# Kernel optimization log

Measured on AMD Instinct MI355X. Metric: run time of the kernel, lower is better.

## Reference

```python
import jax, jax.numpy as jnp
import numpy as np

BITS = 8
KH, KW = 3, 3
STRIDE = (1, 1)
PAD = (1, 1)


def _quantize_signed_symmetric(x, bits=BITS):
    # Per-tensor symmetric quantization: scale = max|x| / qmax, q = clip(round(x/scale)).
    qmax = float(2 ** (bits - 1) - 1)
    scale = jnp.max(jnp.abs(x)) / qmax
    q = jnp.clip(jnp.round(x / scale), -qmax, qmax)
    return q, scale


def _unfold(x, kh, kw, stride, pad):
    # torch.nn.functional.unfold: output [B, C*kh*kw, Hout*Wout], feature order (c, kh, kw).
    B, C, H, W = x.shape
    sh, sw = stride
    ph, pw = pad
    Hout = (H + 2 * ph - kh) // sh + 1
    Wout = (W + 2 * pw - kw) // sw + 1
    xp = jnp.pad(x, ((0, 0), (0, 0), (ph, ph), (pw, pw)))
    patches = []
    for i in range(kh):  # small fixed loop over kernel taps (9 iters)
        for j in range(kw):
            patches.append(
                xp[:, :, i:i + (Hout - 1) * sh + 1:sh, j:j + (Wout - 1) * sw + 1:sw]
            )
    # [B, C, kh*kw, Hout, Wout] -> [B, C*kh*kw, Hout*Wout]
    p = jnp.stack(patches, axis=2)
    return p.reshape(B, C * kh * kw, Hout * Wout), Hout, Wout


def setup_inputs() -> dict:
    key = jax.random.key(0)
    k1, k2, k3 = jax.random.split(key, 3)
    x = jax.random.normal(k1, (8, 32, 224, 224), dtype=jnp.float32)
    weight = jax.random.normal(k2, (32, 32, 3, 3), dtype=jnp.float32)
    bias = jax.random.normal(k3, (32,), dtype=jnp.float32)
    return {"x": x, "weight": weight, "bias": bias}


def reference(x, weight, bias):
    Cout = weight.shape[0]
    B = x.shape[0]
    qw, w_scale = _quantize_signed_symmetric(weight)           # values are exact small ints
    x_unf, Hout, Wout = _unfold(x, KH, KW, STRIDE, PAD)        # [B, K, L], K=Cin*kh*kw
    qx, x_scale = _quantize_signed_symmetric(x_unf)
    qw_flat = qw.reshape(Cout, -1)                             # [Cout, K]
    # Integer GEMM done in fp32: |sum| <= K*127^2 = 288*16129 < 2^24, so exact.
    out = jnp.einsum("ok,bkl->bol", qw_flat, qx)               # [B, Cout, L]
    out = out * (x_scale * w_scale)                            # dequantize
    out = out + bias[None, :, None]
    return out.reshape(B, Cout, Hout, Wout)
```

## Files before the change

### kernel.cpp

```cpp
#include <hip/hip_runtime.h>
#include <hip/hip_bf16.h>
#include <stdint.h>


typedef short short8 __attribute__((ext_vector_type(8)));
typedef float f32x4  __attribute__((ext_vector_type(4)));

#define CIN   32
#define COUT  32
#define HH    224
#define WW    224
#define NB    8
#define QMAXF 127.0f
#define PP    226

#define RED_BLOCKS 1024
#define PF_OFF  16
#define QW_OFF  8192
#define QX_OFF  32768
#define QX_BYTES ((size_t)NB * PP * PP * CIN * 2)


__global__ __launch_bounds__(256) void k_prep(const float* __restrict__ x, int n4,
                                              const float* __restrict__ wgt,
                                              unsigned* __restrict__ ws) {
    const int tid = threadIdx.x;
    __shared__ float red[4];
    if (blockIdx.x < RED_BLOCKS) {
        const float4* x4 = (const float4*)x;
        float m = 0.f;
        for (int i = blockIdx.x * 256 + tid; i < n4; i += RED_BLOCKS * 256) {
            float4 v = x4[i];
            m = fmaxf(m, fmaxf(fmaxf(fabsf(v.x), fabsf(v.y)), fmaxf(fabsf(v.z), fabsf(v.w))));
        }
        #pragma unroll
        for (int off = 32; off >= 1; off >>= 1) m = fmaxf(m, __shfl_xor(m, off));
        if ((tid & 63) == 0) red[tid >> 6] = m;
        __syncthreads();
        if (tid == 0)
            ((float*)ws)[PF_OFF + blockIdx.x] =
                fmaxf(fmaxf(red[0], red[1]), fmaxf(red[2], red[3]));
    } else {
        float m = 0.f;
        for (int i = tid; i < COUT * CIN * 9; i += 256) m = fmaxf(m, fabsf(wgt[i]));
        #pragma unroll
        for (int off = 32; off >= 1; off >>= 1) m = fmaxf(m, __shfl_xor(m, off));
        if ((tid & 63) == 0) red[tid >> 6] = m;
        __syncthreads();
        const float mw = fmaxf(fmaxf(red[0], red[1]), fmaxf(red[2], red[3]));
        const float wscale = mw / QMAXF;
        if (tid == 0) ws[1] = __float_as_uint(wscale);
        ushort* qw = (ushort*)((char*)ws + QW_OFF);
        for (int e = tid; e < COUT * 288; e += 256) {
            const int co = e / 288, k = e % 288;
            const int t = k >> 5, ci = k & 31;
            const int kh = t / 3, kw = t % 3;
            const float v = wgt[((co * CIN + ci) * 3 + kh) * 3 + kw];
            float q = rintf(v / wscale);
            q = fminf(fmaxf(q, -QMAXF), QMAXF);
            qw[e] = (ushort)(__float_as_uint(q) >> 16);
        }
    }
}

__global__ __launch_bounds__(256) void k_quant(const float* __restrict__ x,
                                               unsigned* __restrict__ ws,
                                               ushort* __restrict__ qx) {
    __shared__ float red[4];
    const float* pf = (const float*)ws + PF_OFF;
    float m = 0.f;
    for (int i = threadIdx.x; i < RED_BLOCKS; i += 256) m = fmaxf(m, pf[i]);
    #pragma unroll
    for (int off = 32; off >= 1; off >>= 1) m = fmaxf(m, __shfl_xor(m, off));
    if ((threadIdx.x & 63) == 0) red[threadIdx.x >> 6] = m;
    __syncthreads();
    const float xscale =
        fmaxf(fmaxf(red[0], red[1]), fmaxf(red[2], red[3])) / QMAXF;
    if (blockIdx.x == 0 && threadIdx.x == 0) ws[0] = __float_as_uint(xscale);

    const int total = NB * PP * PP * 4;
    for (int o8 = blockIdx.x * 256 + threadIdx.x; o8 < total; o8 += gridDim.x * 256) {
        const int ci8 = o8 & 3;
        int t = o8 >> 2;
        const int wp = t % PP; t /= PP;
        const int hp = t % PP;
        const int b  = t / PP;
        union { ushort qs[8]; int4 v; } u;
        u.v = make_int4(0, 0, 0, 0);
        if (hp != 0 && hp != PP - 1 && wp != 0 && wp != PP - 1) {
            const float* xp = x + ((size_t)(b * CIN + ci8 * 8) * HH + (hp - 1)) * WW + (wp - 1);
            #pragma unroll
            for (int c = 0; c < 8; ++c) {
                const float v = xp[c * (HH * WW)];
                float q = rintf(v / xscale);
                q = fminf(fmaxf(q, -QMAXF), QMAXF);
                u.qs[c] = (ushort)(__float_as_uint(q) >> 16);
            }
        }
        ((int4*)qx)[o8] = u.v;
    }
}

__global__ __launch_bounds__(256) void k_conv(const ushort* __restrict__ qx,
                                              const ushort* __restrict__ qw,
                                              const float* __restrict__ bias,
                                              const unsigned* __restrict__ ws,
                                              float* __restrict__ out) {
    const int tid  = threadIdx.x;
    const int lane = tid & 63;
    const int wv   = tid >> 6;
    const int w0   = (blockIdx.x % 7) * 32;
    const int hb   = ((blockIdx.x / 7) % 28) * 8;
    const int b    = blockIdx.x / (7 * 28);
    const int h    = hb + wv * 2;
    const int col  = lane & 15;
    const int kgrp = lane >> 4;

    const float s = __uint_as_float(ws[0]) * __uint_as_float(ws[1]);

    short8 afr[9][2];
    #pragma unroll
    for (int t = 0; t < 9; ++t)
        #pragma unroll
        for (int m = 0; m < 2; ++m)
            afr[t][m] = *(const short8*)&qw[((m * 16 + col) * 9 + t) * 32 + kgrp * 8];

    const f32x4 zero = {0.f, 0.f, 0.f, 0.f};
    f32x4 acc[2][2][2];
    #pragma unroll
    for (int o = 0; o < 2; ++o)
        #pragma unroll
        for (int m = 0; m < 2; ++m)
            #pragma unroll
            for (int nt = 0; nt < 2; ++nt) acc[o][m][nt] = zero;

    const ushort* base = qx + (((size_t)b * PP + h) * PP + (w0 + col)) * CIN + kgrp * 8;
    #pragma unroll
    for (int pr = 0; pr < 4; ++pr) {
        #pragma unroll
        for (int kw = 0; kw < 3; ++kw) {
            const ushort* p = base + (pr * PP + kw) * CIN;
            const short8 b0 = *(const short8*)p;
            const short8 b1 = *(const short8*)(p + 16 * CIN);
            if (pr <= 2) {
                const int t = pr * 3 + kw;
                acc[0][0][0] = __builtin_amdgcn_mfma_f32_16x16x32_bf16(afr[t][0], b0, acc[0][0][0], 0, 0, 0);
                acc[0][1][0] = __builtin_amdgcn_mfma_f32_16x16x32_bf16(afr[t][1], b0, acc[0][1][0], 0, 0, 0);
                acc[0][0][1] = __builtin_amdgcn_mfma_f32_16x16x32_bf16(afr[t][0], b1, acc[0][0][1], 0, 0, 0);
                acc[0][1][1] = __builtin_amdgcn_mfma_f32_16x16x32_bf16(afr[t][1], b1, acc[0][1][1], 0, 0, 0);
            }
            if (pr >= 1) {
                const int t = (pr - 1) * 3 + kw;
                acc[1][0][0] = __builtin_amdgcn_mfma_f32_16x16x32_bf16(afr[t][0], b0, acc[1][0][0], 0, 0, 0);
                acc[1][1][0] = __builtin_amdgcn_mfma_f32_16x16x32_bf16(afr[t][1], b0, acc[1][1][0], 0, 0, 0);
                acc[1][0][1] = __builtin_amdgcn_mfma_f32_16x16x32_bf16(afr[t][0], b1, acc[1][0][1], 0, 0, 0);
                acc[1][1][1] = __builtin_amdgcn_mfma_f32_16x16x32_bf16(afr[t][1], b1, acc[1][1][1], 0, 0, 0);
            }
        }
    }

    #pragma unroll
    for (int o = 0; o < 2; ++o) {
        const int hw = (h + o) * WW + w0 + col;
        #pragma unroll
        for (int m = 0; m < 2; ++m)
            #pragma unroll
            for (int r = 0; r < 4; ++r) {
                const int co = m * 16 + kgrp * 4 + r;
                const float bv = bias[co];
                float* op = out + (size_t)(b * COUT + co) * (HH * WW) + hw;
                op[0]  = acc[o][m][0][r] * s + bv;
                op[16] = acc[o][m][1][r] * s + bv;
            }
    }
}

extern "C" void kernel_launch(void* const* d_in, const int* in_sizes, int n_in,
                              void* d_out, int out_size, void* d_ws, size_t ws_size,
                              hipStream_t stream) {
    const float* x    = (const float*)d_in[0];
    const float* wgt  = (const float*)d_in[1];
    const float* bias = (const float*)d_in[2];
    float* out        = (float*)d_out;
    unsigned* ws      = (unsigned*)d_ws;
    ushort* qw        = (ushort*)((char*)d_ws + QW_OFF);
    ushort* qx        = (ushort*)((char*)d_ws + QX_OFF);

    const int n4 = in_sizes[0] / 4;
    k_prep <<<RED_BLOCKS + 1, 256, 0, stream>>>(x, n4, wgt, ws);
    k_quant<<<3200, 256, 0, stream>>>(x, ws, qx);
    k_conv <<<NB * 28 * 7, 256, 0, stream>>>(qx, qw, bias, ws, out);
}
```

Baseline: 145.2 us.

## Switch quantized conv from bf16 MFMA to int8 MFMA with int8 staging

Quantized activations and weights are now stored as int8 instead of bf16, halving the size of the padded intermediate tensor and the bytes the conv kernel reads. The conv inner loop uses 32x32x32 int8 MFMA with int32 accumulators, covering all 32 output channels and 32 columns in one instruction. This replaces four 16x16x32 bf16 MFMAs per tap and output row. The output lane mapping and the quantize packing (16 channels per 16-byte store) are rewritten to match.

After: 132.2 us. 1.1x faster.

```diff
diff --git a/kernel.cpp b/kernel.cpp
--- a/kernel.cpp
+++ b/kernel.cpp
@@ -3,8 +3,8 @@
 #include <stdint.h>
 
 
-typedef short short8 __attribute__((ext_vector_type(8)));
-typedef float f32x4  __attribute__((ext_vector_type(4)));
+typedef int i32x4  __attribute__((ext_vector_type(4)));
+typedef int i32x16 __attribute__((ext_vector_type(16)));
 
 #define CIN   32
 #define COUT  32
@@ -18,7 +18,6 @@
 #define PF_OFF  16
 #define QW_OFF  8192
 #define QX_OFF  32768
-#define QX_BYTES ((size_t)NB * PP * PP * CIN * 2)
 
 
 __global__ __launch_bounds__(256) void k_prep(const float* __restrict__ x, int n4,
@@ -50,7 +49,7 @@
         const float mw = fmaxf(fmaxf(red[0], red[1]), fmaxf(red[2], red[3]));
         const float wscale = mw / QMAXF;
         if (tid == 0) ws[1] = __float_as_uint(wscale);
-        ushort* qw = (ushort*)((char*)ws + QW_OFF);
+        signed char* qw = (signed char*)ws + QW_OFF;
         for (int e = tid; e < COUT * 288; e += 256) {
             const int co = e / 288, k = e % 288;
             const int t = k >> 5, ci = k & 31;
@@ -58,14 +57,14 @@
             const float v = wgt[((co * CIN + ci) * 3 + kh) * 3 + kw];
             float q = rintf(v / wscale);
             q = fminf(fmaxf(q, -QMAXF), QMAXF);
-            qw[e] = (ushort)(__float_as_uint(q) >> 16);
+            qw[e] = (signed char)(int)q;
         }
     }
 }
 
 __global__ __launch_bounds__(256) void k_quant(const float* __restrict__ x,
                                                unsigned* __restrict__ ws,
-                                               ushort* __restrict__ qx) {
+                                               signed char* __restrict__ qx) {
     __shared__ float red[4];
     const float* pf = (const float*)ws + PF_OFF;
     float m = 0.f;
@@ -78,31 +77,32 @@
         fmaxf(fmaxf(red[0], red[1]), fmaxf(red[2], red[3])) / QMAXF;
     if (blockIdx.x == 0 && threadIdx.x == 0) ws[0] = __float_as_uint(xscale);
 
-    const int total = NB * PP * PP * 4;
-    for (int o8 = blockIdx.x * 256 + threadIdx.x; o8 < total; o8 += gridDim.x * 256) {
-        const int ci8 = o8 & 3;
-        int t = o8 >> 2;
+    const int total = NB * PP * PP * 2;
+    for (int o16 = blockIdx.x * 256 + threadIdx.x; o16 < total; o16 += gridDim.x * 256) {
+        const int half = o16 & 1;
+        int t = o16 >> 1;
         const int wp = t % PP; t /= PP;
         const int hp = t % PP;
         const int b  = t / PP;
-        union { ushort qs[8]; int4 v; } u;
+        union { signed char c[16]; int4 v; } u;
         u.v = make_int4(0, 0, 0, 0);
         if (hp != 0 && hp != PP - 1 && wp != 0 && wp != PP - 1) {
-            const float* xp = x + ((size_t)(b * CIN + ci8 * 8) * HH + (hp - 1)) * WW + (wp - 1);
+            const float* xp =
+                x + ((size_t)(b * CIN + half * 16) * HH + (hp - 1)) * WW + (wp - 1);
             #pragma unroll
-            for (int c = 0; c < 8; ++c) {
+            for (int c = 0; c < 16; ++c) {
                 const float v = xp[c * (HH * WW)];
                 float q = rintf(v / xscale);
                 q = fminf(fmaxf(q, -QMAXF), QMAXF);
-                u.qs[c] = (ushort)(__float_as_uint(q) >> 16);
+                u.c[c] = (signed char)(int)q;
             }
         }
-        ((int4*)qx)[o8] = u.v;
+        ((int4*)qx)[o16] = u.v;
     }
 }
 
-__global__ __launch_bounds__(256) void k_conv(const ushort* __restrict__ qx,
-                                              const ushort* __restrict__ qw,
+__global__ __launch_bounds__(256) void k_conv(const signed char* __restrict__ qx,
+                                              const signed char* __restrict__ qw,
                                               const float* __restrict__ bias,
                                               const unsigned* __restrict__ ws,
                                               float* __restrict__ out) {
@@ -113,65 +113,41 @@
     const int hb   = ((blockIdx.x / 7) % 28) * 8;
     const int b    = blockIdx.x / (7 * 28);
     const int h    = hb + wv * 2;
-    const int col  = lane & 15;
-    const int kgrp = lane >> 4;
+    const int col  = lane & 31;
+    const int hi   = lane >> 5;
 
     const float s = __uint_as_float(ws[0]) * __uint_as_float(ws[1]);
 
-    short8 afr[9][2];
+    i32x4 afr[9];
     #pragma unroll
     for (int t = 0; t < 9; ++t)
-        #pragma unroll
-        for (int m = 0; m < 2; ++m)
-            afr[t][m] = *(const short8*)&qw[((m * 16 + col) * 9 + t) * 32 + kgrp * 8];
+        afr[t] = *(const i32x4*)&qw[col * 288 + t * 32 + hi * 16];
 
-    const f32x4 zero = {0.f, 0.f, 0.f, 0.f};
-    f32x4 acc[2][2][2];
-    #pragma unroll
-    for (int o = 0; o < 2; ++o)
-        #pragma unroll
-        for (int m = 0; m < 2; ++m)
-            #pragma unroll
-            for (int nt = 0; nt < 2; ++nt) acc[o][m][nt] = zero;
+    i32x16 acc0 = {0,0,0,0,0,0,0,0,0,0,0,0,0,0,0,0};
+    i32x16 acc1 = {0,0,0,0,0,0,0,0,0,0,0,0,0,0,0,0};
 
-    const ushort* base = qx + (((size_t)b * PP + h) * PP + (w0 + col)) * CIN + kgrp * 8;
+    const signed char* base =
+        qx + (((size_t)b * PP + h) * PP + (w0 + col)) * CIN + hi * 16;
     #pragma unroll
     for (int pr = 0; pr < 4; ++pr) {
         #pragma unroll
         for (int kw = 0; kw < 3; ++kw) {
-            const ushort* p = base + (pr * PP + kw) * CIN;
-            const short8 b0 = *(const short8*)p;
-            const short8 b1 = *(const short8*)(p + 16 * CIN);
-            if (pr <= 2) {
-                const int t = pr * 3 + kw;
-                acc[0][0][0] = __builtin_amdgcn_mfma_f32_16x16x32_bf16(afr[t][0], b0, acc[0][0][0], 0, 0, 0);
-                acc[0][1][0] = __builtin_amdgcn_mfma_f32_16x16x32_bf16(afr[t][1], b0, acc[0][1][0], 0, 0, 0);
-                acc[0][0][1] = __builtin_amdgcn_mfma_f32_16x16x32_bf16(afr[t][0], b1, acc[0][0][1], 0, 0, 0);
-                acc[0][1][1] = __builtin_amdgcn_mfma_f32_16x16x32_bf16(afr[t][1], b1, acc[0][1][1], 0, 0, 0);
-            }
-            if (pr >= 1) {
-                const int t = (pr - 1) * 3 + kw;
-                acc[1][0][0] = __builtin_amdgcn_mfma_f32_16x16x32_bf16(afr[t][0], b0, acc[1][0][0], 0, 0, 0);
-                acc[1][1][0] = __builtin_amdgcn_mfma_f32_16x16x32_bf16(afr[t][1], b0, acc[1][1][0], 0, 0, 0);
-                acc[1][0][1] = __builtin_amdgcn_mfma_f32_16x16x32_bf16(afr[t][0], b1, acc[1][0][1], 0, 0, 0);
-                acc[1][1][1] = __builtin_amdgcn_mfma_f32_16x16x32_bf16(afr[t][1], b1, acc[1][1][1], 0, 0, 0);
-            }
+            const i32x4 bf = *(const i32x4*)(base + (pr * PP + kw) * CIN);
+            if (pr <= 2)
+                acc0 = __builtin_amdgcn_mfma_i32_32x32x32_i8(afr[pr * 3 + kw], bf, acc0, 0, 0, 0);
+            if (pr >= 1)
+                acc1 = __builtin_amdgcn_mfma_i32_32x32x32_i8(afr[(pr - 1) * 3 + kw], bf, acc1, 0, 0, 0);
         }
     }
 
+    const size_t hw0 = (size_t)h * WW + w0 + col;
     #pragma unroll
-    for (int o = 0; o < 2; ++o) {
-        const int hw = (h + o) * WW + w0 + col;
-        #pragma unroll
-        for (int m = 0; m < 2; ++m)
-            #pragma unroll
-            for (int r = 0; r < 4; ++r) {
-                const int co = m * 16 + kgrp * 4 + r;
-                const float bv = bias[co];
-                float* op = out + (size_t)(b * COUT + co) * (HH * WW) + hw;
-                op[0]  = acc[o][m][0][r] * s + bv;
-                op[16] = acc[o][m][1][r] * s + bv;
-            }
+    for (int r = 0; r < 16; ++r) {
+        const int co = (r & 3) + 8 * (r >> 2) + 4 * hi;
+        const float bv = bias[co];
+        float* op = out + (size_t)(b * COUT + co) * (HH * WW) + hw0;
+        op[0]  = (float)acc0[r] * s + bv;
+        op[WW] = (float)acc1[r] * s + bv;
     }
 }
 
@@ -183,8 +159,8 @@
     const float* bias = (const float*)d_in[2];
     float* out        = (float*)d_out;
     unsigned* ws      = (unsigned*)d_ws;
-    ushort* qw        = (ushort*)((char*)d_ws + QW_OFF);
-    ushort* qx        = (ushort*)((char*)d_ws + QX_OFF);
+    const signed char* qw = (const signed char*)d_ws + QW_OFF;
+    signed char* qx       = (signed char*)d_ws + QX_OFF;
 
     const int n4 = in_sizes[0] / 4;
     k_prep <<<RED_BLOCKS + 1, 256, 0, stream>>>(x, n4, wgt, ws);
```
